# Kernel tuning notes

Hardware: AMD Instinct MI355X
Metric: run time of the kernel (lower is better)

## Reference

```python
import jax, jax.numpy as jnp
import numpy as np

N = 50000      # nodes
E = 800000     # edges
CIN = 128
CH = 128
COUT = 64
EPS = 1e-5     # BatchNorm eps


def setup_inputs() -> dict:
    key = jax.random.key(0)
    ks = jax.random.split(key, 16)
    s = 0.1  # weight scale for numerical stability
    return {
        "x": jax.random.normal(ks[0], (N, CIN), jnp.float32),
        "edge_index": jax.random.randint(ks[1], (2, E), 0, N, jnp.int32),
        "edge_weights": jax.random.uniform(ks[2], (E,), jnp.float32),
        "w1": jax.random.normal(ks[3], (CIN, CH), jnp.float32) * s,
        "b1": jnp.zeros((CH,), jnp.float32),
        "bn1_g": jnp.ones((CH,), jnp.float32),
        "bn1_b": jnp.zeros((CH,), jnp.float32),
        "bn1_m": jax.random.normal(ks[4], (CH,), jnp.float32) * 0.1,
        "bn1_v": jax.random.uniform(ks[5], (CH,), jnp.float32) + 0.5,
        "conv_ws": jax.random.normal(ks[6], (2, CH, CH), jnp.float32) * s,
        "conv_bs": jnp.zeros((2, CH), jnp.float32),
        "bns_g": jnp.ones((2, CH), jnp.float32),
        "bns_b": jnp.zeros((2, CH), jnp.float32),
        "bns_m": jax.random.normal(ks[7], (2, CH), jnp.float32) * 0.1,
        "bns_v": jax.random.uniform(ks[8], (2, CH), jnp.float32) + 0.5,
        "lin1_w": jax.random.normal(ks[9], (CH, CH), jnp.float32) * s,
        "lin1_b": jnp.zeros((CH,), jnp.float32),
        "lin2_w": jax.random.normal(ks[10], (CH, COUT), jnp.float32) * s,
        "lin2_b": jnp.zeros((COUT,), jnp.float32),
    }


def _bn(h, g, b, m, v):
    # BatchNorm1d in eval mode: running statistics
    return (h - m) * jax.lax.rsqrt(v + EPS) * g + b


def _gcn(h, w, b, src, dst, norm, n):
    # GCNConv: out[dst] += norm_e * (h @ W)[src]  (self loops already in src/dst)
    h = h @ w
    msg = h[src] * norm[:, None]                 # [E+N, CH]
    return jax.ops.segment_sum(msg, dst, num_segments=n) + b


def reference(x, edge_index, edge_weights, w1, b1, bn1_g, bn1_b, bn1_m, bn1_v,
              conv_ws, conv_bs, bns_g, bns_b, bns_m, bns_v,
              lin1_w, lin1_b, lin2_w, lin2_b):
    n = x.shape[0]
    loop = jnp.arange(n, dtype=edge_index.dtype)
    src = jnp.concatenate([edge_index[0], loop])
    dst = jnp.concatenate([edge_index[1], loop])
    ew = jnp.concatenate([edge_weights, jnp.ones((n,), edge_weights.dtype)])
    # symmetric degree normalization (PyG gcn_norm)
    deg = jax.ops.segment_sum(ew, dst, num_segments=n)
    dis = jnp.where(deg > 0, jax.lax.rsqrt(deg), 0.0)
    norm = dis[src] * ew * dis[dst]

    lrelu = jax.nn.leaky_relu  # slope 0.01, matches F.leaky_relu default
    h = lrelu(_bn(_gcn(x, w1, b1, src, dst, norm, n), bn1_g, bn1_b, bn1_m, bn1_v))
    for i in range(conv_ws.shape[0]):
        h = lrelu(_bn(_gcn(h, conv_ws[i], conv_bs[i], src, dst, norm, n),
                      bns_g[i], bns_b[i], bns_m[i], bns_v[i]) + h)
    h = lrelu(h @ lin1_w + lin1_b)
    # dropout is identity in eval mode
    return h @ lin2_w + lin2_b
```

## Files before the change

kernel.cpp:

```cpp
#include <hip/hip_runtime.h>
#include <hip/hip_bf16.h>


constexpr int   NN    = 50000;
constexpr int   EE    = 800000;
constexpr int   CH    = 128;
constexpr int   SLOTS = 64;
constexpr int   NBUK  = 782;
constexpr int   RCAP  = 2048;
constexpr int   EPB   = 4096;
constexpr float EPS   = 1e-5f;

typedef __attribute__((ext_vector_type(8))) short bf16x8;
typedef __attribute__((ext_vector_type(4))) float f32x4;
typedef unsigned long long u64;
typedef unsigned short u16;

__device__ inline u16 f2bf_rne(float f) {
  unsigned u = __float_as_uint(f);
  unsigned r = u + 0x7fffu + ((u >> 16) & 1u);
  return (u16)(r >> 16);
}
__device__ inline float bf2f(unsigned h16) {
  return __uint_as_float(h16 << 16);
}


__global__ __launch_bounds__(256) void bin_kernel(const int* __restrict__ ei,
                                                  const float* __restrict__ ew,
                                                  unsigned* __restrict__ gcur,
                                                  u64* __restrict__ bins) {
  __shared__ unsigned cnt[NBUK];
  __shared__ unsigned base[NBUK];
  const int tid = threadIdx.x;
  for (int b = tid; b < NBUK; b += 256) cnt[b] = 0;
  __syncthreads();
  const int e0 = blockIdx.x * EPB;
  unsigned pk[16]; u16 bkt[16]; u16 rnk[16]; unsigned char dl[16];
  #pragma unroll
  for (int i = 0; i < 16; i++) {
    int e = e0 + i * 256 + tid;
    if (e < EE) {
      int s = ei[e], d = ei[EE + e];
      float w = ew[e];
      bkt[i] = (u16)(d >> 6);
      dl[i]  = (unsigned char)(d & 63);
      pk[i]  = ((unsigned)f2bf_rne(w) << 16) | (unsigned)s;
      rnk[i] = (u16)atomicAdd(&cnt[bkt[i]], 1u);
    } else bkt[i] = 0xffffu;
  }
  __syncthreads();
  for (int b = tid; b < NBUK; b += 256) {
    unsigned c = cnt[b];
    base[b] = c ? atomicAdd(&gcur[b * 16], c) : 0u;
  }
  __syncthreads();
  #pragma unroll
  for (int i = 0; i < 16; i++) {
    if (bkt[i] == 0xffffu) continue;
    unsigned pos = base[bkt[i]] + rnk[i];
    if (pos < RCAP)
      bins[(size_t)bkt[i] * RCAP + pos] = ((u64)dl[i] << 32) | pk[i];
  }
}


__global__ __launch_bounds__(256) void scatter_kernel(const unsigned* __restrict__ gcur,
                                                      const u64* __restrict__ bins,
                                                      unsigned* __restrict__ ell,
                                                      float* __restrict__ dis) {
  __shared__ unsigned rank[64];
  __shared__ float    wsum[64];
  const int b   = blockIdx.x;
  const int tid = threadIdx.x;
  if (tid < 64) { rank[tid] = 1u; wsum[tid] = 0.f; }
  __syncthreads();
  unsigned cnt = gcur[b * 16];
  if (cnt > RCAP) cnt = RCAP;
  const u64* src = bins + (size_t)b * RCAP;
  for (unsigned i = tid; i < cnt; i += 256) {
    u64 v = src[i];
    unsigned pk = (unsigned)v;
    unsigned dl = (unsigned)(v >> 32);
    unsigned r = atomicAdd(&rank[dl], 1u);
    if (r < SLOTS)
      ell[((size_t)(b * 64 + dl)) * SLOTS + r] = pk;
    atomicAdd(&wsum[dl], bf2f(pk >> 16));
  }
  __syncthreads();
  if (tid < 64) {
    int node = b * 64 + tid;
    if (node < NN) {
      unsigned c = rank[tid];
      if (c > SLOTS) c = SLOTS;
      ell[(size_t)node * SLOTS] = c;
      dis[node] = rsqrtf(1.0f + wsum[tid]);
    }
  }
}

constexpr int NB_WZ = (73728 + 255) / 256;

__global__ void wswz_kernel(
    const float* __restrict__ w1, const float* __restrict__ bn1_g, const float* __restrict__ bn1_v,
    const float* __restrict__ conv_ws, const float* __restrict__ bns_g, const float* __restrict__ bns_v,
    const float* __restrict__ lin1_w, const float* __restrict__ lin2_w,
    u16* __restrict__ w1h, u16* __restrict__ w1l,
    u16* __restrict__ c0h, u16* __restrict__ c0l,
    u16* __restrict__ c1h, u16* __restrict__ c1l,
    u16* __restrict__ l1h, u16* __restrict__ l1l,
    u16* __restrict__ l2h, u16* __restrict__ l2l)
{
  int idx = blockIdx.x * 256 + threadIdx.x;
  const float* W; const float* g = nullptr; const float* v = nullptr;
  u16 *hi, *lo; int CO = 128; int local;
  if      (idx < 16384) { W = w1;              g = bn1_g;     v = bn1_v;     hi = w1h; lo = w1l; local = idx; }
  else if (idx < 32768) { W = conv_ws;         g = bns_g;     v = bns_v;     hi = c0h; lo = c0l; local = idx - 16384; }
  else if (idx < 49152) { W = conv_ws + 16384; g = bns_g+128; v = bns_v+128; hi = c1h; lo = c1l; local = idx - 32768; }
  else if (idx < 65536) { W = lin1_w;                                        hi = l1h; lo = l1l; local = idx - 49152; }
  else if (idx < 73728) { W = lin2_w;                                        hi = l2h; lo = l2l; local = idx - 65536; CO = 64; }
  else return;
  int k = local / CO, n = local % CO;
  float w = W[local];
  if (g) w *= g[n] * rsqrtf(v[n] + EPS);
  int NCT = CO / 16;
  int kchunk = k >> 5, kin = k & 31, quad = kin >> 3, j = kin & 7;
  int ct = n >> 4, l = (quad << 4) | (n & 15);
  size_t pos = ((size_t)(kchunk * NCT + ct) * 64 + l) * 8 + j;
  u16 h = f2bf_rne(w);
  hi[pos] = h;
  lo[pos] = f2bf_rne(w - bf2f(h));
}

template<int CO, int EPI, bool OUT_BF16, bool A_BF16, bool SCALE>
__global__ __launch_bounds__(256) void mgemm_kernel(
    const void* __restrict__ Ain,
    const u16* __restrict__ Whi, const u16* __restrict__ Wlo,
    const float* __restrict__ bias, const float* __restrict__ dis,
    void* __restrict__ Cout)
{
  constexpr int NCT = CO / 16;
  __shared__ float lds[64][CO + 4];

  const int tid  = threadIdx.x;
  const int wave = tid >> 6;
  const int lane = tid & 63;
  const int quad = lane >> 4;
  const int mrow = lane & 15;
  const int row0 = blockIdx.x * 64;

  int arow = row0 + wave * 16 + mrow;
  if (arow >= NN) arow = NN - 1;

  bf16x8 ahi[4], alo[4];
  if constexpr (A_BF16) {
    const u16* Ar = (const u16*)Ain + (size_t)arow * CH;
    #pragma unroll
    for (int c = 0; c < 4; c++)
      ahi[c] = *(const bf16x8*)(Ar + c * 32 + quad * 8);
  } else {
    const float* Ar = (const float*)Ain + (size_t)arow * CH;
    #pragma unroll
    for (int c = 0; c < 4; c++) {
      int off = c * 32 + quad * 8;
      float4 f0 = *(const float4*)(Ar + off);
      float4 f1 = *(const float4*)(Ar + off + 4);
      float f[8] = {f0.x, f0.y, f0.z, f0.w, f1.x, f1.y, f1.z, f1.w};
      #pragma unroll
      for (int j = 0; j < 8; j++) {
        u16 h = f2bf_rne(f[j]);
        ahi[c][j] = (short)h;
        alo[c][j] = (short)f2bf_rne(f[j] - bf2f(h));
      }
    }
  }

  f32x4 acc[NCT];
  #pragma unroll
  for (int t = 0; t < NCT; t++) acc[t] = (f32x4){0.f, 0.f, 0.f, 0.f};

  #pragma unroll
  for (int c = 0; c < 4; c++) {
    #pragma unroll
    for (int t = 0; t < NCT; t++) {
      size_t base = ((size_t)(c * NCT + t) * 64 + lane) * 8;
      bf16x8 bh = *(const bf16x8*)(Whi + base);
      bf16x8 bl = *(const bf16x8*)(Wlo + base);
      acc[t] = __builtin_amdgcn_mfma_f32_16x16x32_bf16(ahi[c], bh, acc[t], 0, 0, 0);
      if constexpr (!A_BF16)
        acc[t] = __builtin_amdgcn_mfma_f32_16x16x32_bf16(alo[c], bh, acc[t], 0, 0, 0);
      acc[t] = __builtin_amdgcn_mfma_f32_16x16x32_bf16(ahi[c], bl, acc[t], 0, 0, 0);
    }
  }

  #pragma unroll
  for (int t = 0; t < NCT; t++)
    #pragma unroll
    for (int r = 0; r < 4; r++)
      lds[wave * 16 + quad * 4 + r][t * 16 + mrow] = acc[t][r];
  __syncthreads();

  constexpr int TOTE = 64 * CO / 4;
  #pragma unroll
  for (int i = tid; i < TOTE; i += 256) {
    int row = (i * 4) / CO;
    int col = (i * 4) % CO;
    int grow = row0 + row;
    if (grow >= NN) continue;
    float rs = 1.0f;
    if constexpr (SCALE) rs = dis[grow];
    const float* lp = &lds[row][col];
    float o[4];
    #pragma unroll
    for (int q = 0; q < 4; q++) {
      float x = lp[q];
      if constexpr (EPI >= 1) {
        x += bias[col + q];
        if constexpr (EPI == 1) x = x > 0.f ? x : 0.01f * x;
      }
      if constexpr (SCALE) x *= rs;
      o[q] = x;
    }
    if constexpr (OUT_BF16) {
      u16* cp = (u16*)Cout + (size_t)grow * CO + col;
      unsigned p0 = ((unsigned)f2bf_rne(o[1]) << 16) | f2bf_rne(o[0]);
      unsigned p1 = ((unsigned)f2bf_rne(o[3]) << 16) | f2bf_rne(o[2]);
      *(uint2*)cp = make_uint2(p0, p1);
    } else {
      float* cp = (float*)Cout + (size_t)grow * CO + col;
      *(float4*)cp = make_float4(o[0], o[1], o[2], o[3]);
    }
  }
}

__global__ __launch_bounds__(256) void linf_kernel(
    const u16* __restrict__ Ain,
    const u16* __restrict__ l1h, const u16* __restrict__ l1l,
    const float* __restrict__ b1,
    const u16* __restrict__ l2h, const u16* __restrict__ l2l,
    const float* __restrict__ b2, float* __restrict__ out)
{
  __shared__ float lds[64][CH + 4];
  const int tid  = threadIdx.x;
  const int wave = tid >> 6;
  const int lane = tid & 63;
  const int quad = lane >> 4;
  const int mrow = lane & 15;
  const int row0 = blockIdx.x * 64;

  int arow = row0 + wave * 16 + mrow;
  if (arow >= NN) arow = NN - 1;

  bf16x8 a1[4];
  {
    const u16* Ar = Ain + (size_t)arow * CH;
    #pragma unroll
    for (int c = 0; c < 4; c++)
      a1[c] = *(const bf16x8*)(Ar + c * 32 + quad * 8);
  }
  f32x4 acc[8];
  #pragma unroll
  for (int t = 0; t < 8; t++) acc[t] = (f32x4){0.f, 0.f, 0.f, 0.f};
  #pragma unroll
  for (int c = 0; c < 4; c++) {
    #pragma unroll
    for (int t = 0; t < 8; t++) {
      size_t base = ((size_t)(c * 8 + t) * 64 + lane) * 8;
      bf16x8 bh = *(const bf16x8*)(l1h + base);
      bf16x8 bl = *(const bf16x8*)(l1l + base);
      acc[t] = __builtin_amdgcn_mfma_f32_16x16x32_bf16(a1[c], bh, acc[t], 0, 0, 0);
      acc[t] = __builtin_amdgcn_mfma_f32_16x16x32_bf16(a1[c], bl, acc[t], 0, 0, 0);
    }
  }
  #pragma unroll
  for (int t = 0; t < 8; t++) {
    float bb = b1[t * 16 + mrow];
    #pragma unroll
    for (int r = 0; r < 4; r++) {
      float x = acc[t][r] + bb;
      x = x > 0.f ? x : 0.01f * x;
      lds[wave * 16 + quad * 4 + r][t * 16 + mrow] = x;
    }
  }
  __syncthreads();

  f32x4 acc2[4];
  #pragma unroll
  for (int t = 0; t < 4; t++) acc2[t] = (f32x4){0.f, 0.f, 0.f, 0.f};
  const int lrow = wave * 16 + mrow;
  #pragma unroll
  for (int c = 0; c < 4; c++) {
    bf16x8 ahi, alo;
    const float* lp = &lds[lrow][c * 32 + quad * 8];
    float4 f0 = *(const float4*)lp;
    float4 f1 = *(const float4*)(lp + 4);
    float f[8] = {f0.x, f0.y, f0.z, f0.w, f1.x, f1.y, f1.z, f1.w};
    #pragma unroll
    for (int j = 0; j < 8; j++) {
      u16 h = f2bf_rne(f[j]);
      ahi[j] = (short)h;
      alo[j] = (short)f2bf_rne(f[j] - bf2f(h));
    }
    #pragma unroll
    for (int t = 0; t < 4; t++) {
      size_t base = ((size_t)(c * 4 + t) * 64 + lane) * 8;
      bf16x8 bh = *(const bf16x8*)(l2h + base);
      bf16x8 bl = *(const bf16x8*)(l2l + base);
      acc2[t] = __builtin_amdgcn_mfma_f32_16x16x32_bf16(ahi, bh, acc2[t], 0, 0, 0);
      acc2[t] = __builtin_amdgcn_mfma_f32_16x16x32_bf16(alo, bh, acc2[t], 0, 0, 0);
      acc2[t] = __builtin_amdgcn_mfma_f32_16x16x32_bf16(ahi, bl, acc2[t], 0, 0, 0);
    }
  }
  #pragma unroll
  for (int t = 0; t < 4; t++) {
    float bb = b2[t * 16 + mrow];
    #pragma unroll
    for (int r = 0; r < 4; r++) {
      int grow = row0 + wave * 16 + quad * 4 + r;
      if (grow < NN)
        out[(size_t)grow * 64 + t * 16 + mrow] = acc2[t][r] + bb;
    }
  }
}

template<bool RES>
__global__ __launch_bounds__(256) void agg_kernel(
    const u16* __restrict__ hw,
    const unsigned* __restrict__ ell, const float* __restrict__ dis,
    const float* __restrict__ conv_b, const float* __restrict__ g,
    const float* __restrict__ bb, const float* __restrict__ m,
    const float* __restrict__ v,
    const u16* __restrict__ res, u16* __restrict__ out)
{
  int node = (blockIdx.x * blockDim.x + threadIdx.x) >> 6;
  int lane = threadIdx.x & 63;
  if (node >= NN) return;

  unsigned myword = ell[(size_t)node * SLOTS + lane];
  int cnt = __shfl((int)myword, 0);
  if (cnt > SLOTS) cnt = SLOTS;

  unsigned us = *(const unsigned*)(hw + (size_t)node * CH + lane * 2);
  float ax = bf2f(us & 0xffffu);
  float ay = bf2f(us >> 16);

  int j = 1;
  for (; j + 4 <= cnt; j += 4) {
    unsigned e0 = (unsigned)__shfl((int)myword, j);
    unsigned e1 = (unsigned)__shfl((int)myword, j + 1);
    unsigned e2 = (unsigned)__shfl((int)myword, j + 2);
    unsigned e3 = (unsigned)__shfl((int)myword, j + 3);
    unsigned u0 = *(const unsigned*)(hw + (size_t)(e0 & 0xffffu) * CH + lane * 2);
    unsigned u1 = *(const unsigned*)(hw + (size_t)(e1 & 0xffffu) * CH + lane * 2);
    unsigned u2 = *(const unsigned*)(hw + (size_t)(e2 & 0xffffu) * CH + lane * 2);
    unsigned u3 = *(const unsigned*)(hw + (size_t)(e3 & 0xffffu) * CH + lane * 2);
    float w0 = bf2f(e0 >> 16), w1 = bf2f(e1 >> 16);
    float w2 = bf2f(e2 >> 16), w3 = bf2f(e3 >> 16);
    ax = fmaf(w0, bf2f(u0 & 0xffffu), ax); ay = fmaf(w0, bf2f(u0 >> 16), ay);
    ax = fmaf(w1, bf2f(u1 & 0xffffu), ax); ay = fmaf(w1, bf2f(u1 >> 16), ay);
    ax = fmaf(w2, bf2f(u2 & 0xffffu), ax); ay = fmaf(w2, bf2f(u2 >> 16), ay);
    ax = fmaf(w3, bf2f(u3 & 0xffffu), ax); ay = fmaf(w3, bf2f(u3 >> 16), ay);
  }
  for (; j < cnt; j++) {
    unsigned e0 = (unsigned)__shfl((int)myword, j);
    unsigned u0 = *(const unsigned*)(hw + (size_t)(e0 & 0xffffu) * CH + lane * 2);
    float w0 = bf2f(e0 >> 16);
    ax = fmaf(w0, bf2f(u0 & 0xffffu), ax); ay = fmaf(w0, bf2f(u0 >> 16), ay);
  }

  float disd = dis[node];
  int c = lane * 2;
  float sc0 = g[c]     * rsqrtf(v[c]     + EPS);
  float sc1 = g[c + 1] * rsqrtf(v[c + 1] + EPS);
  float y0 = ax * disd + (conv_b[c]     - m[c])     * sc0 + bb[c];
  float y1 = ay * disd + (conv_b[c + 1] - m[c + 1]) * sc1 + bb[c + 1];
  if constexpr (RES) {
    unsigned r = *(const unsigned*)(res + (size_t)node * CH + c);
    y0 += bf2f(r & 0xffffu);
    y1 += bf2f(r >> 16);
  }
  y0 = y0 > 0.f ? y0 : 0.01f * y0;
  y1 = y1 > 0.f ? y1 : 0.01f * y1;
  *(unsigned*)(out + (size_t)node * CH + c) =
      ((unsigned)f2bf_rne(y1) << 16) | f2bf_rne(y0);
}


extern "C" void kernel_launch(void* const* d_in, const int* in_sizes, int n_in,
                              void* d_out, int out_size, void* d_ws, size_t ws_size,
                              hipStream_t stream) {
  const float* x       = (const float*)d_in[0];
  const int*   ei      = (const int*)  d_in[1];
  const float* ew      = (const float*)d_in[2];
  const float* w1      = (const float*)d_in[3];
  const float* b1      = (const float*)d_in[4];
  const float* bn1_g   = (const float*)d_in[5];
  const float* bn1_b   = (const float*)d_in[6];
  const float* bn1_m   = (const float*)d_in[7];
  const float* bn1_v   = (const float*)d_in[8];
  const float* conv_ws = (const float*)d_in[9];
  const float* conv_bs = (const float*)d_in[10];
  const float* bns_g   = (const float*)d_in[11];
  const float* bns_b   = (const float*)d_in[12];
  const float* bns_m   = (const float*)d_in[13];
  const float* bns_v   = (const float*)d_in[14];
  const float* lin1_w  = (const float*)d_in[15];
  const float* lin1_b  = (const float*)d_in[16];
  const float* lin2_w  = (const float*)d_in[17];
  const float* lin2_b  = (const float*)d_in[18];
  float* out = (float*)d_out;

  size_t off = 0;
  auto alloc = [&](size_t elems) -> void* {
    void* p = (char*)d_ws + off * 4;
    off += (elems + 3) & ~(size_t)3;
    return p;
  };
  unsigned* gcur = (unsigned*)alloc(NBUK * 16);
  u64*      bins = (u64*)     alloc((size_t)NBUK * RCAP * 2);
  unsigned* ell  = (unsigned*)alloc((size_t)NN * SLOTS);
  float*    dis  = (float*)   alloc(NN);
  u16*      hwb  = (u16*)     alloc((size_t)NN * CH / 2);
  u16*      hA   = (u16*)     alloc((size_t)NN * CH / 2);
  u16* w1h = (u16*)alloc(CH * CH / 2); u16* w1l = (u16*)alloc(CH * CH / 2);
  u16* c0h = (u16*)alloc(CH * CH / 2); u16* c0l = (u16*)alloc(CH * CH / 2);
  u16* c1h = (u16*)alloc(CH * CH / 2); u16* c1l = (u16*)alloc(CH * CH / 2);
  u16* l1h = (u16*)alloc(CH * CH / 2); u16* l1l = (u16*)alloc(CH * CH / 2);
  u16* l2h = (u16*)alloc(CH * 64 / 2); u16* l2l = (u16*)alloc(CH * 64 / 2);

  const int nb_bin  = (EE + EPB - 1) / EPB;
  const int nb_gemm = (NN + 63) / 64;
  const int nb_agg  = (NN * 64 + 255) / 256;
  dim3 B(256);

  hipMemsetAsync(gcur, 0, NBUK * 16 * sizeof(unsigned), stream);
  bin_kernel    <<<nb_bin, B, 0, stream>>>(ei, ew, gcur, bins);
  scatter_kernel<<<NBUK,   B, 0, stream>>>(gcur, bins, ell, dis);

  wswz_kernel<<<NB_WZ, B, 0, stream>>>(w1, bn1_g, bn1_v, conv_ws, bns_g, bns_v,
      lin1_w, lin2_w, w1h, w1l, c0h, c0l, c1h, c1l, l1h, l1l, l2h, l2l);

  mgemm_kernel<128, 0, true, false, true><<<nb_gemm, B, 0, stream>>>(x, w1h, w1l, nullptr, dis, hwb);
  agg_kernel<false><<<nb_agg, B, 0, stream>>>(hwb, ell, dis,
      b1, bn1_g, bn1_b, bn1_m, bn1_v, nullptr, hA);

  mgemm_kernel<128, 0, true, true, true><<<nb_gemm, B, 0, stream>>>(hA, c0h, c0l, nullptr, dis, hwb);
  agg_kernel<true><<<nb_agg, B, 0, stream>>>(hwb, ell, dis,
      conv_bs, bns_g, bns_b, bns_m, bns_v, hA, hA);

  mgemm_kernel<128, 0, true, true, true><<<nb_gemm, B, 0, stream>>>(hA, c1h, c1l, nullptr, dis, hwb);
  agg_kernel<true><<<nb_agg, B, 0, stream>>>(hwb, ell, dis,
      conv_bs + CH, bns_g + CH, bns_b + CH, bns_m + CH, bns_v + CH, hA, hA);

  linf_kernel<<<nb_gemm, B, 0, stream>>>(hA, l1h, l1l, lin1_b, l2h, l2l, lin2_b, out);
}
```

Baseline: 329.3 us.

## Gather 16-byte rows per lane group in aggregation and precompute fused BN bias

The aggregation kernel now splits each 64-lane wave into four groups of 16 lanes. Each group gathers a different neighbor row using 16-byte vector loads covering 8 channels per lane, and the four partial sums are combined with cross-lane xor shuffles. The BatchNorm bias and shift terms are folded into one effective bias per layer inside the weight-swizzle kernel, which removes per-node rsqrt and parameter loads. The goal is more bytes in flight per gather instruction and fewer memory operations. In exchange it adds a reduction step and lets only a quarter of the lanes do the epilogue.

```diff
diff --git a/kernel.cpp b/kernel.cpp
--- a/kernel.cpp
+++ b/kernel.cpp
@@ -99,27 +99,42 @@
   }
 }
 
-constexpr int NB_WZ = (73728 + 255) / 256;
+constexpr int NB_WZ = (73728 + 384 + 255) / 256;
 
 __global__ void wswz_kernel(
     const float* __restrict__ w1, const float* __restrict__ bn1_g, const float* __restrict__ bn1_v,
     const float* __restrict__ conv_ws, const float* __restrict__ bns_g, const float* __restrict__ bns_v,
     const float* __restrict__ lin1_w, const float* __restrict__ lin2_w,
+    const float* __restrict__ b1, const float* __restrict__ bn1_b, const float* __restrict__ bn1_m,
+    const float* __restrict__ conv_bs, const float* __restrict__ bns_b, const float* __restrict__ bns_m,
     u16* __restrict__ w1h, u16* __restrict__ w1l,
     u16* __restrict__ c0h, u16* __restrict__ c0l,
     u16* __restrict__ c1h, u16* __restrict__ c1l,
     u16* __restrict__ l1h, u16* __restrict__ l1l,
-    u16* __restrict__ l2h, u16* __restrict__ l2l)
+    u16* __restrict__ l2h, u16* __restrict__ l2l,
+    float* __restrict__ beff)
 {
   int idx = blockIdx.x * 256 + threadIdx.x;
+  if (idx >= 73728) {
+    int r = idx - 73728;
+    if (r >= 384) return;
+    int l = r >> 7, c = r & 127;
+    float bc, gg, bb, mm, vv;
+    if (l == 0) { bc = b1[c]; gg = bn1_g[c]; bb = bn1_b[c]; mm = bn1_m[c]; vv = bn1_v[c]; }
+    else {
+      int o = (l - 1) * 128 + c;
+      bc = conv_bs[o]; gg = bns_g[o]; bb = bns_b[o]; mm = bns_m[o]; vv = bns_v[o];
+    }
+    beff[r] = (bc - mm) * gg * rsqrtf(vv + EPS) + bb;
+    return;
+  }
   const float* W; const float* g = nullptr; const float* v = nullptr;
   u16 *hi, *lo; int CO = 128; int local;
   if      (idx < 16384) { W = w1;              g = bn1_g;     v = bn1_v;     hi = w1h; lo = w1l; local = idx; }
   else if (idx < 32768) { W = conv_ws;         g = bns_g;     v = bns_v;     hi = c0h; lo = c0l; local = idx - 16384; }
   else if (idx < 49152) { W = conv_ws + 16384; g = bns_g+128; v = bns_v+128; hi = c1h; lo = c1l; local = idx - 32768; }
   else if (idx < 65536) { W = lin1_w;                                        hi = l1h; lo = l1l; local = idx - 49152; }
-  else if (idx < 73728) { W = lin2_w;                                        hi = l2h; lo = l2l; local = idx - 65536; CO = 64; }
-  else return;
+  else                  { W = lin2_w;                                        hi = l2h; lo = l2l; local = idx - 65536; CO = 64; }
   int k = local / CO, n = local % CO;
   float w = W[local];
   if (g) w *= g[n] * rsqrtf(v[n] + EPS);
@@ -327,62 +342,75 @@
 __global__ __launch_bounds__(256) void agg_kernel(
     const u16* __restrict__ hw,
     const unsigned* __restrict__ ell, const float* __restrict__ dis,
-    const float* __restrict__ conv_b, const float* __restrict__ g,
-    const float* __restrict__ bb, const float* __restrict__ m,
-    const float* __restrict__ v,
+    const float* __restrict__ beff,
     const u16* __restrict__ res, u16* __restrict__ out)
 {
   int node = (blockIdx.x * blockDim.x + threadIdx.x) >> 6;
   int lane = threadIdx.x & 63;
   if (node >= NN) return;
+  const int sub = lane & 15;
+  const int grp = lane >> 4;
 
   unsigned myword = ell[(size_t)node * SLOTS + lane];
   int cnt = __shfl((int)myword, 0);
   if (cnt > SLOTS) cnt = SLOTS;
 
-  unsigned us = *(const unsigned*)(hw + (size_t)node * CH + lane * 2);
-  float ax = bf2f(us & 0xffffu);
-  float ay = bf2f(us >> 16);
-
-  int j = 1;
-  for (; j + 4 <= cnt; j += 4) {
-    unsigned e0 = (unsigned)__shfl((int)myword, j);
-    unsigned e1 = (unsigned)__shfl((int)myword, j + 1);
-    unsigned e2 = (unsigned)__shfl((int)myword, j + 2);
-    unsigned e3 = (unsigned)__shfl((int)myword, j + 3);
-    unsigned u0 = *(const unsigned*)(hw + (size_t)(e0 & 0xffffu) * CH + lane * 2);
-    unsigned u1 = *(const unsigned*)(hw + (size_t)(e1 & 0xffffu) * CH + lane * 2);
-    unsigned u2 = *(const unsigned*)(hw + (size_t)(e2 & 0xffffu) * CH + lane * 2);
-    unsigned u3 = *(const unsigned*)(hw + (size_t)(e3 & 0xffffu) * CH + lane * 2);
-    float w0 = bf2f(e0 >> 16), w1 = bf2f(e1 >> 16);
-    float w2 = bf2f(e2 >> 16), w3 = bf2f(e3 >> 16);
-    ax = fmaf(w0, bf2f(u0 & 0xffffu), ax); ay = fmaf(w0, bf2f(u0 >> 16), ay);
-    ax = fmaf(w1, bf2f(u1 & 0xffffu), ax); ay = fmaf(w1, bf2f(u1 >> 16), ay);
-    ax = fmaf(w2, bf2f(u2 & 0xffffu), ax); ay = fmaf(w2, bf2f(u2 >> 16), ay);
-    ax = fmaf(w3, bf2f(u3 & 0xffffu), ax); ay = fmaf(w3, bf2f(u3 >> 16), ay);
-  }
-  for (; j < cnt; j++) {
-    unsigned e0 = (unsigned)__shfl((int)myword, j);
-    unsigned u0 = *(const unsigned*)(hw + (size_t)(e0 & 0xffffu) * CH + lane * 2);
-    float w0 = bf2f(e0 >> 16);
-    ax = fmaf(w0, bf2f(u0 & 0xffffu), ax); ay = fmaf(w0, bf2f(u0 >> 16), ay);
-  }
-
-  float disd = dis[node];
-  int c = lane * 2;
-  float sc0 = g[c]     * rsqrtf(v[c]     + EPS);
-  float sc1 = g[c + 1] * rsqrtf(v[c + 1] + EPS);
-  float y0 = ax * disd + (conv_b[c]     - m[c])     * sc0 + bb[c];
-  float y1 = ay * disd + (conv_b[c + 1] - m[c + 1]) * sc1 + bb[c + 1];
-  if constexpr (RES) {
-    unsigned r = *(const unsigned*)(res + (size_t)node * CH + c);
-    y0 += bf2f(r & 0xffffu);
-    y1 += bf2f(r >> 16);
-  }
-  y0 = y0 > 0.f ? y0 : 0.01f * y0;
-  y1 = y1 > 0.f ? y1 : 0.01f * y1;
-  *(unsigned*)(out + (size_t)node * CH + c) =
-      ((unsigned)f2bf_rne(y1) << 16) | f2bf_rne(y0);
+  float a[8] = {0.f, 0.f, 0.f, 0.f, 0.f, 0.f, 0.f, 0.f};
+
+  for (int j = 0; j < cnt; j += 8) {
+    int j0 = j + grp, j1 = j + 4 + grp;
+    unsigned e0 = (unsigned)__shfl((int)myword, j0);
+    unsigned e1 = (unsigned)__shfl((int)myword, j1 & 63);
+    float    w0 = (j0 == 0) ? 1.0f : bf2f(e0 >> 16);
+    unsigned s0 = (j0 == 0) ? (unsigned)node : (e0 & 0xffffu);
+    float    w1 = bf2f(e1 >> 16);
+    unsigned s1 = e1 & 0xffffu;
+    if (j0 >= cnt) { w0 = 0.f; s0 = (unsigned)node; }
+    if (j1 >= cnt) { w1 = 0.f; s1 = (unsigned)node; }
+    uint4 h0 = *(const uint4*)(hw + (size_t)s0 * CH + sub * 8);
+    uint4 h1 = *(const uint4*)(hw + (size_t)s1 * CH + sub * 8);
+    a[0] = fmaf(w0, bf2f(h0.x & 0xffffu), a[0]); a[1] = fmaf(w0, bf2f(h0.x >> 16), a[1]);
+    a[2] = fmaf(w0, bf2f(h0.y & 0xffffu), a[2]); a[3] = fmaf(w0, bf2f(h0.y >> 16), a[3]);
+    a[4] = fmaf(w0, bf2f(h0.z & 0xffffu), a[4]); a[5] = fmaf(w0, bf2f(h0.z >> 16), a[5]);
+    a[6] = fmaf(w0, bf2f(h0.w & 0xffffu), a[6]); a[7] = fmaf(w0, bf2f(h0.w >> 16), a[7]);
+    a[0] = fmaf(w1, bf2f(h1.x & 0xffffu), a[0]); a[1] = fmaf(w1, bf2f(h1.x >> 16), a[1]);
+    a[2] = fmaf(w1, bf2f(h1.y & 0xffffu), a[2]); a[3] = fmaf(w1, bf2f(h1.y >> 16), a[3]);
+    a[4] = fmaf(w1, bf2f(h1.z & 0xffffu), a[4]); a[5] = fmaf(w1, bf2f(h1.z >> 16), a[5]);
+    a[6] = fmaf(w1, bf2f(h1.w & 0xffffu), a[6]); a[7] = fmaf(w1, bf2f(h1.w >> 16), a[7]);
+  }
+
+  #pragma unroll
+  for (int k = 0; k < 8; k++) {
+    a[k] += __shfl_xor(a[k], 16);
+    a[k] += __shfl_xor(a[k], 32);
+  }
+
+  if (grp == 0) {
+    float disd = dis[node];
+    int c = sub * 8;
+    float4 be0 = *(const float4*)(beff + c);
+    float4 be1 = *(const float4*)(beff + c + 4);
+    float y[8];
+    y[0] = a[0] * disd + be0.x; y[1] = a[1] * disd + be0.y;
+    y[2] = a[2] * disd + be0.z; y[3] = a[3] * disd + be0.w;
+    y[4] = a[4] * disd + be1.x; y[5] = a[5] * disd + be1.y;
+    y[6] = a[6] * disd + be1.z; y[7] = a[7] * disd + be1.w;
+    if constexpr (RES) {
+      uint4 r = *(const uint4*)(res + (size_t)node * CH + c);
+      y[0] += bf2f(r.x & 0xffffu); y[1] += bf2f(r.x >> 16);
+      y[2] += bf2f(r.y & 0xffffu); y[3] += bf2f(r.y >> 16);
+      y[4] += bf2f(r.z & 0xffffu); y[5] += bf2f(r.z >> 16);
+      y[6] += bf2f(r.w & 0xffffu); y[7] += bf2f(r.w >> 16);
+    }
+    #pragma unroll
+    for (int k = 0; k < 8; k++) y[k] = y[k] > 0.f ? y[k] : 0.01f * y[k];
+    uint4 o;
+    o.x = ((unsigned)f2bf_rne(y[1]) << 16) | f2bf_rne(y[0]);
+    o.y = ((unsigned)f2bf_rne(y[3]) << 16) | f2bf_rne(y[2]);
+    o.z = ((unsigned)f2bf_rne(y[5]) << 16) | f2bf_rne(y[4]);
+    o.w = ((unsigned)f2bf_rne(y[7]) << 16) | f2bf_rne(y[6]);
+    *(uint4*)(out + (size_t)node * CH + c) = o;
+  }
 }
 
 
@@ -420,6 +448,7 @@
   u64*      bins = (u64*)     alloc((size_t)NBUK * RCAP * 2);
   unsigned* ell  = (unsigned*)alloc((size_t)NN * SLOTS);
   float*    dis  = (float*)   alloc(NN);
+  float*    beff = (float*)   alloc(3 * CH);
   u16*      hwb  = (u16*)     alloc((size_t)NN * CH / 2);
   u16*      hA   = (u16*)     alloc((size_t)NN * CH / 2);
   u16* w1h = (u16*)alloc(CH * CH / 2); u16* w1l = (u16*)alloc(CH * CH / 2);
@@ -438,19 +467,17 @@
   scatter_kernel<<<NBUK,   B, 0, stream>>>(gcur, bins, ell, dis);
 
   wswz_kernel<<<NB_WZ, B, 0, stream>>>(w1, bn1_g, bn1_v, conv_ws, bns_g, bns_v,
-      lin1_w, lin2_w, w1h, w1l, c0h, c0l, c1h, c1l, l1h, l1l, l2h, l2l);
+      lin1_w, lin2_w, b1, bn1_b, bn1_m, conv_bs, bns_b, bns_m,
+      w1h, w1l, c0h, c0l, c1h, c1l, l1h, l1l, l2h, l2l, beff);
 
   mgemm_kernel<128, 0, true, false, true><<<nb_gemm, B, 0, stream>>>(x, w1h, w1l, nullptr, dis, hwb);
-  agg_kernel<false><<<nb_agg, B, 0, stream>>>(hwb, ell, dis,
-      b1, bn1_g, bn1_b, bn1_m, bn1_v, nullptr, hA);
+  agg_kernel<false><<<nb_agg, B, 0, stream>>>(hwb, ell, dis, beff, nullptr, hA);
 
   mgemm_kernel<128, 0, true, true, true><<<nb_gemm, B, 0, stream>>>(hA, c0h, c0l, nullptr, dis, hwb);
-  agg_kernel<true><<<nb_agg, B, 0, stream>>>(hwb, ell, dis,
-      conv_bs, bns_g, bns_b, bns_m, bns_v, hA, hA);
+  agg_kernel<true><<<nb_agg, B, 0, stream>>>(hwb, ell, dis, beff + CH, hA, hA);
 
   mgemm_kernel<128, 0, true, true, true><<<nb_gemm, B, 0, stream>>>(hA, c1h, c1l, nullptr, dis, hwb);
-  agg_kernel<true><<<nb_agg, B, 0, stream>>>(hwb, ell, dis,
-      conv_bs + CH, bns_g + CH, bns_b + CH, bns_m + CH, bns_v + CH, hA, hA);
+  agg_kernel<true><<<nb_agg, B, 0, stream>>>(hwb, ell, dis, beff + 2 * CH, hA, hA);
 
   linf_kernel<<<nb_gemm, B, 0, stream>>>(hA, l1h, l1l, lin1_b, l2h, l2l, lin2_b, out);
 }
```

Result: no change. 324.3 us (-1.5%).
